# Optimization experiments

Hardware: AMD Instinct MI355X
Metric: run time of the kernel (lower is better)

## Reference

```python
import jax, jax.numpy as jnp
import numpy as np

VMIN, VMAX, N = -5.0, 5.0, 100          # InvertiblePWL defaults
INT_LEN = (VMAX - VMIN) / (N - 1)       # bin width
B, D = 2_000_000, 16


def setup_inputs() -> dict:
    key = jax.random.key(0)
    k1, k2, k3, k4 = jax.random.split(key, 4)
    eps = jax.random.normal(k1, (B, D), dtype=jnp.float32)
    # small-magnitude adjacency so (I - A) is well-conditioned
    A = 0.05 * jax.random.normal(k2, (D, D), dtype=jnp.float32)
    # per-dim PWL params: torch inits p = randn(n+1)/5, b = randn(1) + vmin
    p = jax.random.normal(k3, (D, N + 1), dtype=jnp.float32) / 5.0
    b = jax.random.normal(k4, (D,), dtype=jnp.float32) + VMIN
    return {"eps": eps, "A": A, "p": p, "b": b}


def _pwl_forward(z, p, b):
    """Vectorized InvertiblePWL.forward over all d dims at once.
    z: [B, d]; p: [d, N+1]; b: [d]  ->  out: [B, d]
    """
    points = jnp.linspace(VMIN, VMAX, N, dtype=z.dtype)  # [N], same for all dims
    # delta_h is detached in torch (p[1:n] slice) -> stop_gradient
    delta_h = jax.lax.stop_gradient(INT_LEN * (jnp.exp(p[:, 1:N]) + 0.001))  # [d, N-1]
    # serial cumsum in torch == prefix-sum: delta_bias[0]=b, delta_bias[i+1]=delta_bias[i]+delta_h[i]
    delta_bias = b[:, None] + jnp.concatenate(
        [jnp.zeros((p.shape[0], 1), z.dtype), jnp.cumsum(delta_h, axis=1)], axis=1
    )  # [d, N]
    # index = sum(eps >= points) == searchsorted(points, z, 'right'), in [0, N]
    index = jnp.searchsorted(points, z, side="right")          # [B, d]
    sp_idx = jnp.maximum(index - 1, 0)                          # clamp at 0
    db = jnp.take_along_axis(delta_bias.T, sp_idx, axis=0)      # [B, d]
    sp = jax.lax.stop_gradient(points[sp_idx])                  # start points, detached
    w = jnp.exp(jnp.take_along_axis(p.T, index, axis=0)) + 0.001  # [B, d]
    return (z - sp) * w + db


def reference(eps, A, p, b):
    d = A.shape[0]
    # SCM.inv_cal: z = eps @ inv(I - A)
    adj_normalized = jnp.linalg.inv(jnp.eye(d, dtype=A.dtype) - A)
    z = eps @ adj_normalized                                    # [B, d]
    # SCM.prior_nlr: per-dim InvertiblePWL
    return _pwl_forward(z, p, b)
```

## Files before the change

kernel.cpp:

```cpp
#include <hip/hip_runtime.h>
#include <math.h>

#define D_DIM 16
#define N_PTS 100
#define VMIN_F (-5.0f)
#define INT_LEN_F (10.0f / 99.0f)
#define INV_INT_LEN_F (99.0f / 10.0f)

__global__ void scm_setup(const float* __restrict__ A,
                          const float* __restrict__ p,
                          const float* __restrict__ b,
                          float* __restrict__ Minv,
                          float2* __restrict__ Ctab) {
    __shared__ double aug[16][33];
    __shared__ float db_s[16][N_PTS];
    __shared__ int piv;
    const int t = threadIdx.x;

    if (t < 16) {
        #pragma unroll
        for (int j = 0; j < 16; j++) {
            aug[t][j]      = (t == j ? 1.0 : 0.0) - (double)A[t * 16 + j];
            aug[t][16 + j] = (t == j ? 1.0 : 0.0);
        }
    }
    __syncthreads();

    for (int k = 0; k < 16; k++) {
        if (t == 0) {
            int pr = k; double best = fabs(aug[k][k]);
            for (int i = k + 1; i < 16; i++) {
                double v = fabs(aug[i][k]);
                if (v > best) { best = v; pr = i; }
            }
            piv = pr;
        }
        __syncthreads();
        const int pr = piv;
        if (pr != k && t < 32) {
            double tmp = aug[k][t]; aug[k][t] = aug[pr][t]; aug[pr][t] = tmp;
        }
        __syncthreads();
        const double pivval = aug[k][k];
        __syncthreads();
        if (t < 32) aug[k][t] = aug[k][t] / pivval;
        __syncthreads();
        if (t < 16 && t != k) {
            const double f = aug[t][k];
            #pragma unroll
            for (int j = 0; j < 32; j++) aug[t][j] -= f * aug[k][j];
        }
        __syncthreads();
    }

    if (t < 16) {
        #pragma unroll
        for (int j = 0; j < 16; j++) Minv[t * 16 + j] = (float)aug[t][16 + j];
    }

    if (t < 16) {
        float acc = b[t];
        db_s[t][0] = acc;
        for (int i = 1; i < N_PTS; i++) {
            acc += INT_LEN_F * (expf(p[t * (N_PTS + 1) + i]) + 0.001f);
            db_s[t][i] = acc;
        }
    }
    __syncthreads();

    for (int i = t; i < 16 * (N_PTS + 1); i += blockDim.x) {
        const int d   = i / (N_PTS + 1);
        const int idx = i - d * (N_PTS + 1);
        const int spi = idx > 0 ? idx - 1 : 0;
        float2 c;
        c.x = expf(p[i]) + 0.001f;
        c.y = db_s[d][spi];
        Ctab[i] = c;
    }
}

__global__ __launch_bounds__(256) void scm_main(
        const float* __restrict__ eps,
        const float* __restrict__ Minv,
        const float2* __restrict__ Ctab,
        float* __restrict__ out, int B) {
    __shared__ float2 sC[16 * (N_PTS + 1)];

    const int t = threadIdx.x;
    const int row = blockIdx.x * 256 + t;

    float4 c0 = {0,0,0,0}, c1 = {0,0,0,0}, c2 = {0,0,0,0}, c3 = {0,0,0,0};
    if (row < B) {
        const float4* erow = (const float4*)(eps + (size_t)row * 16);
        c0 = erow[0]; c1 = erow[1]; c2 = erow[2]; c3 = erow[3];
    }

    for (int i = t; i < 16 * (N_PTS + 1); i += 256) sC[i] = Ctab[i];
    __syncthreads();

    if (row >= B) return;

    const float e[16] = {c0.x, c0.y, c0.z, c0.w, c1.x, c1.y, c1.z, c1.w,
                         c2.x, c2.y, c2.z, c2.w, c3.x, c3.y, c3.z, c3.w};

    float z[16];
    #pragma unroll
    for (int d = 0; d < 16; d++) z[d] = 0.0f;

    #pragma unroll
    for (int k = 0; k < 16; k++) {
        const float ek = e[k];
        #pragma unroll
        for (int d = 0; d < 16; d++) {
            z[d] = fmaf(ek, Minv[k * 16 + d], z[d]);
        }
    }

    float o[16];
    #pragma unroll
    for (int d = 0; d < 16; d++) {
        const float zd = z[d];
        const float tt = (zd - VMIN_F) * INV_INT_LEN_F;
        int idx = (int)floorf(tt) + 1;
        idx = min(max(idx, 0), N_PTS);
        const int sp_idx = max(idx - 1, 0);
        const float sp = VMIN_F + (float)sp_idx * INT_LEN_F;
        const float2 c = sC[d * (N_PTS + 1) + idx];
        o[d] = fmaf(zd - sp, c.x, c.y);
    }

    float4* orow = (float4*)(out + (size_t)row * 16);
    orow[0] = make_float4(o[0],  o[1],  o[2],  o[3]);
    orow[1] = make_float4(o[4],  o[5],  o[6],  o[7]);
    orow[2] = make_float4(o[8],  o[9],  o[10], o[11]);
    orow[3] = make_float4(o[12], o[13], o[14], o[15]);
}

extern "C" void kernel_launch(void* const* d_in, const int* in_sizes, int n_in,
                              void* d_out, int out_size, void* d_ws, size_t ws_size,
                              hipStream_t stream) {
    const float* eps = (const float*)d_in[0];
    const float* A   = (const float*)d_in[1];
    const float* p   = (const float*)d_in[2];
    const float* b   = (const float*)d_in[3];
    float* out = (float*)d_out;

    const int B = in_sizes[0] / D_DIM;

    float*  ws   = (float*)d_ws;
    float*  Minv = ws;
    float2* Ctab = (float2*)(ws + 256);

    scm_setup<<<1, 256, 0, stream>>>(A, p, b, Minv, Ctab);

    const int blocks = (B + 255) / 256;
    scm_main<<<blocks, 256, 0, stream>>>(eps, Minv, Ctab, out, B);
}
```

Baseline: 285.9 us.

## Split each row across four lanes with DPP broadcast and grid-stride prefetch loop

Each row is now handled by a quad of four lanes, each loading one float4 so global loads and stores are fully coalesced. The 16 input values are shared within the quad via DPP quad-perm broadcasts, and each lane computes four output columns with its Minv slice held in registers. A persistent grid-stride loop with a fixed block count and a one-iteration prefetch replaces the one-row-per-thread launch. This trades the strided per-thread 64-byte accesses for DPP shuffles and more loop overhead, and it cuts the per-block table staging into LDS.

Measured after the change: 270.6 us. 1.06x faster.

```diff
diff --git a/kernel.cpp b/kernel.cpp
--- a/kernel.cpp
+++ b/kernel.cpp
@@ -79,7 +79,15 @@
     }
 }
 
-__global__ __launch_bounds__(256) void scm_main(
+template <int J>
+__device__ __forceinline__ float dpp_bcast(float x) {
+    constexpr int ctrl = J | (J << 2) | (J << 4) | (J << 6);
+    int xi = __builtin_bit_cast(int, x);
+    int r  = __builtin_amdgcn_mov_dpp(xi, ctrl, 0xf, 0xf, true);
+    return __builtin_bit_cast(float, r);
+}
+
+__global__ __launch_bounds__(256, 4) void scm_main(
         const float* __restrict__ eps,
         const float* __restrict__ Minv,
         const float2* __restrict__ Ctab,
@@ -87,53 +95,68 @@
     __shared__ float2 sC[16 * (N_PTS + 1)];
 
     const int t = threadIdx.x;
-    const int row = blockIdx.x * 256 + t;
-
-    float4 c0 = {0,0,0,0}, c1 = {0,0,0,0}, c2 = {0,0,0,0}, c3 = {0,0,0,0};
-    if (row < B) {
-        const float4* erow = (const float4*)(eps + (size_t)row * 16);
-        c0 = erow[0]; c1 = erow[1]; c2 = erow[2]; c3 = erow[3];
-    }
+    const int q = t & 3;
 
     for (int i = t; i < 16 * (N_PTS + 1); i += 256) sC[i] = Ctab[i];
+
+    float4 Mcol[16];
+    #pragma unroll
+    for (int k = 0; k < 16; k++)
+        Mcol[k] = *(const float4*)(Minv + k * 16 + 4 * q);
+
     __syncthreads();
 
-    if (row >= B) return;
+    const long total  = (long)B * 4;
+    const long stride = (long)gridDim.x * 256;
+    long f4 = (long)blockIdx.x * 256 + t;
 
-    const float e[16] = {c0.x, c0.y, c0.z, c0.w, c1.x, c1.y, c1.z, c1.w,
-                         c2.x, c2.y, c2.z, c2.w, c3.x, c3.y, c3.z, c3.w};
+    const float4* in4  = (const float4*)eps;
+    float4*       out4 = (float4*)out;
 
-    float z[16];
-    #pragma unroll
-    for (int d = 0; d < 16; d++) z[d] = 0.0f;
+    float4 cur = make_float4(0.f, 0.f, 0.f, 0.f);
+    if (f4 < total) cur = in4[f4];
 
-    #pragma unroll
-    for (int k = 0; k < 16; k++) {
-        const float ek = e[k];
+    for (; f4 < total; f4 += stride) {
+        const long nf4 = f4 + stride;
+        float4 nxt = make_float4(0.f, 0.f, 0.f, 0.f);
+        if (nf4 < total) nxt = in4[nf4];
+
+        float e[16];
+        e[0]  = dpp_bcast<0>(cur.x); e[1]  = dpp_bcast<0>(cur.y);
+        e[2]  = dpp_bcast<0>(cur.z); e[3]  = dpp_bcast<0>(cur.w);
+        e[4]  = dpp_bcast<1>(cur.x); e[5]  = dpp_bcast<1>(cur.y);
+        e[6]  = dpp_bcast<1>(cur.z); e[7]  = dpp_bcast<1>(cur.w);
+        e[8]  = dpp_bcast<2>(cur.x); e[9]  = dpp_bcast<2>(cur.y);
+        e[10] = dpp_bcast<2>(cur.z); e[11] = dpp_bcast<2>(cur.w);
+        e[12] = dpp_bcast<3>(cur.x); e[13] = dpp_bcast<3>(cur.y);
+        e[14] = dpp_bcast<3>(cur.z); e[15] = dpp_bcast<3>(cur.w);
+
+        float z0 = 0.f, z1 = 0.f, z2 = 0.f, z3 = 0.f;
         #pragma unroll
-        for (int d = 0; d < 16; d++) {
-            z[d] = fmaf(ek, Minv[k * 16 + d], z[d]);
+        for (int k = 0; k < 16; k++) {
+            z0 = fmaf(e[k], Mcol[k].x, z0);
+            z1 = fmaf(e[k], Mcol[k].y, z1);
+            z2 = fmaf(e[k], Mcol[k].z, z2);
+            z3 = fmaf(e[k], Mcol[k].w, z3);
         }
+
+        float zv[4] = {z0, z1, z2, z3};
+        float o[4];
+        #pragma unroll
+        for (int i = 0; i < 4; i++) {
+            const float zd = zv[i];
+            const float tt = (zd - VMIN_F) * INV_INT_LEN_F;
+            int idx = (int)floorf(tt) + 1;
+            idx = min(max(idx, 0), N_PTS);
+            const int sp_idx = max(idx - 1, 0);
+            const float sp = VMIN_F + (float)sp_idx * INT_LEN_F;
+            const float2 c = sC[(4 * q + i) * (N_PTS + 1) + idx];
+            o[i] = fmaf(zd - sp, c.x, c.y);
+        }
+
+        out4[f4] = make_float4(o[0], o[1], o[2], o[3]);
+        cur = nxt;
     }
-
-    float o[16];
-    #pragma unroll
-    for (int d = 0; d < 16; d++) {
-        const float zd = z[d];
-        const float tt = (zd - VMIN_F) * INV_INT_LEN_F;
-        int idx = (int)floorf(tt) + 1;
-        idx = min(max(idx, 0), N_PTS);
-        const int sp_idx = max(idx - 1, 0);
-        const float sp = VMIN_F + (float)sp_idx * INT_LEN_F;
-        const float2 c = sC[d * (N_PTS + 1) + idx];
-        o[d] = fmaf(zd - sp, c.x, c.y);
-    }
-
-    float4* orow = (float4*)(out + (size_t)row * 16);
-    orow[0] = make_float4(o[0],  o[1],  o[2],  o[3]);
-    orow[1] = make_float4(o[4],  o[5],  o[6],  o[7]);
-    orow[2] = make_float4(o[8],  o[9],  o[10], o[11]);
-    orow[3] = make_float4(o[12], o[13], o[14], o[15]);
 }
 
 extern "C" void kernel_launch(void* const* d_in, const int* in_sizes, int n_in,
@@ -153,6 +176,9 @@
 
     scm_setup<<<1, 256, 0, stream>>>(A, p, b, Minv, Ctab);
 
-    const int blocks = (B + 255) / 256;
+    long total_f4 = (long)B * 4;
+    int blocks = (int)((total_f4 + 255) / 256);
+    if (blocks > 2048) blocks = 2048;
+    if (blocks < 1) blocks = 1;
     scm_main<<<blocks, 256, 0, stream>>>(eps, Minv, Ctab, out, B);
 }
```
